# Kernel tuning notes

Hardware: AMD Instinct MI355X
Metric: run time of the kernel (lower is better)

Reference implementation:

```python
import jax, jax.numpy as jnp
import numpy as np

LN_EPS = 1e-5
BOUNDARY_ID = 0  # boundary_ids = {space_id} = {0}


def setup_inputs() -> dict:
    key = jax.random.key(0)
    k1, k2, k3 = jax.random.split(key, 3)
    B, T, D = 16, 8192, 256
    x = jax.random.normal(k1, (B, T, D), dtype=jnp.float32)
    input_ids = jax.random.randint(k2, (B, T), 0, 8, dtype=jnp.int64)
    W_proj = jax.random.normal(k3, (D, D), dtype=jnp.float32) / np.sqrt(D)
    b_proj = jnp.zeros((D,), dtype=jnp.float32)
    gamma = jnp.ones((D,), dtype=jnp.float32)
    beta = jnp.zeros((D,), dtype=jnp.float32)
    return {"x": x, "input_ids": input_ids, "W_proj": W_proj,
            "b_proj": b_proj, "gamma": gamma, "beta": beta}


def _pool(x, input_ids):
    # Boundary-defined segment mean pooling, vectorized via segment_sum.
    B, T, D = x.shape
    boundary = input_ids == BOUNDARY_ID                       # [B,T]
    nonb = ~boundary
    # A segment starts at a non-boundary token at t=0 or right after a boundary.
    prev_is_b = jnp.concatenate(
        [jnp.ones((B, 1), dtype=bool), boundary[:, :-1]], axis=1)
    start = nonb & prev_is_b
    seg = jnp.cumsum(start.astype(jnp.int32), axis=1) - 1     # seg idx per token
    MAXW = T  # static upper bound on number of segments (jit-safe padding)
    row_off = jnp.arange(B, dtype=jnp.int32)[:, None] * MAXW
    dump = B * MAXW  # boundary tokens go to a dummy segment, dropped below
    flat_ids = jnp.where(nonb, seg + row_off, dump).reshape(-1)
    sums = jax.ops.segment_sum(x.reshape(-1, D), flat_ids,
                               num_segments=B * MAXW + 1)[:-1]
    counts = jax.ops.segment_sum(jnp.ones((B * T,), x.dtype), flat_ids,
                                 num_segments=B * MAXW + 1)[:-1]
    sums = sums.reshape(B, MAXW, D)
    counts = counts.reshape(B, MAXW)
    mask = (counts > 0).astype(x.dtype)                       # [B,MAXW]
    padded = sums / jnp.maximum(counts, 1.0)[..., None]       # zeros where empty
    return padded, mask


def reference(x, input_ids, W_proj, b_proj, gamma, beta):
    padded, mask = _pool(x, input_ids)
    out = jnp.einsum('bwd,ed->bwe', padded, W_proj) + b_proj  # nn.Linear
    mu = jnp.mean(out, axis=-1, keepdims=True)
    var = jnp.mean(jnp.square(out - mu), axis=-1, keepdims=True)
    out = (out - mu) * jax.lax.rsqrt(var + LN_EPS) * gamma + beta
    return out, mask
```

## Files before the change

kernel.cpp:

```cpp
#include <hip/hip_runtime.h>
#include <hip/hip_bf16.h>
#include <math.h>

#define BB 16
#define TT 8192
#define DD 256
#define MAXSEG 4096
#define RPB 8
#define LN_EPS 1e-5f

typedef float vfloat4 __attribute__((ext_vector_type(4)));

__device__ inline float4 f4add(float4 a, float4 b) {
    a.x += b.x; a.y += b.y; a.z += b.z; a.w += b.w; return a;
}

__global__ __launch_bounds__(1024) void setup_kernel(
    const int* __restrict__ ids, const float* __restrict__ W,
    const float* __restrict__ bp, const float* __restrict__ gamma,
    const float* __restrict__ beta, int* __restrict__ counts,
    int* __restrict__ seg_start, int* __restrict__ nseg_g,
    float* __restrict__ mask_out, float* __restrict__ Wt,
    float* __restrict__ ln_empty) {
    __shared__ int wtot_s[16];
    __shared__ int wtot_n[16];
    __shared__ int segs[MAXSEG];
    __shared__ int pvals[MAXSEG];

    int tid = threadIdx.x;
    int lane = tid & 63;
    int wv = tid >> 6;

    if (blockIdx.x >= BB) {
        int bi = blockIdx.x - BB;
        if (bi < 64) {
            int d = bi * 4 + (tid >> 8);
            int e = tid & 255;
            Wt[d * DD + e] = W[e * DD + d];
        } else if (wv == 0) {
            int e0 = lane * 4;
            float4 v = *(const float4*)(bp + e0);
            float s = v.x + v.y + v.z + v.w;
            float sq = v.x * v.x + v.y * v.y + v.z * v.z + v.w * v.w;
#pragma unroll
            for (int o = 32; o > 0; o >>= 1) {
                s += __shfl_down(s, o);
                sq += __shfl_down(sq, o);
            }
            s = __shfl(s, 0);
            sq = __shfl(sq, 0);
            float mu = s * (1.f / (float)DD);
            float var = sq * (1.f / (float)DD) - mu * mu;
            float rs = rsqrtf(fmaxf(var, 0.f) + LN_EPS);
            float4 ge = *(const float4*)(gamma + e0);
            float4 be = *(const float4*)(beta + e0);
            float4 o4;
            o4.x = (v.x - mu) * rs * ge.x + be.x;
            o4.y = (v.y - mu) * rs * ge.y + be.y;
            o4.z = (v.z - mu) * rs * ge.z + be.z;
            o4.w = (v.w - mu) * rs * ge.w + be.w;
            *(float4*)(ln_empty + e0) = o4;
        }
        return;
    }

    const int TPT = 8;
    int b = blockIdx.x;
    const int* row = ids + b * TT;
    int t0 = tid * TPT;

    int4 q0 = ((const int4*)(row + t0))[0];
    int4 q1 = ((const int4*)(row + t0))[1];
    int v[TPT] = {q0.x, q0.y, q0.z, q0.w, q1.x, q1.y, q1.z, q1.w};
    int prev = (tid == 0) ? 0 : row[t0 - 1];

    bool nb[TPT], st[TPT];
    int cstart = 0, cnon = 0;
#pragma unroll
    for (int j = 0; j < TPT; ++j) {
        nb[j] = (v[j] != 0);
        int pv = (j == 0) ? prev : v[j - 1];
        st[j] = nb[j] && (pv == 0);
        cstart += st[j] ? 1 : 0;
        cnon += nb[j] ? 1 : 0;
    }

    int ss = cstart, sn = cnon;
#pragma unroll
    for (int o = 1; o < 64; o <<= 1) {
        int us = __shfl_up(ss, o);
        int un = __shfl_up(sn, o);
        if (lane >= o) { ss += us; sn += un; }
    }
    if (lane == 63) { wtot_s[wv] = ss; wtot_n[wv] = sn; }
    __syncthreads();

    int bs = 0, bn = 0, tot_s = 0, tot_n = 0;
#pragma unroll
    for (int j = 0; j < 16; ++j) {
        int a = wtot_s[j], c = wtot_n[j];
        if (j < wv) { bs += a; bn += c; }
        tot_s += a; tot_n += c;
    }
    bs += ss - cstart;
    bn += sn - cnon;

#pragma unroll
    for (int j = 0; j < TPT; ++j) {
        if (st[j]) { segs[bs] = t0 + j; pvals[bs] = bn; bs++; }
        bn += nb[j] ? 1 : 0;
    }
    __syncthreads();

    int ns = tot_s;
    for (int w = tid; w < TT; w += 1024) {
        int c = 0;
        if (w < ns) {
            int pe = (w + 1 < ns) ? pvals[w + 1] : tot_n;
            c = pe - pvals[w];
            seg_start[b * TT + w] = segs[w];
        }
        counts[b * TT + w] = c;
        mask_out[b * TT + w] = (w < ns) ? 1.0f : 0.0f;
    }
    if (tid == 0) nseg_g[b] = ns;
}

__global__ __launch_bounds__(256) void work_kernel(
    const float* __restrict__ x, const float* __restrict__ Wt,
    const float* __restrict__ bp, const float* __restrict__ gamma,
    const float* __restrict__ beta, const int* __restrict__ counts,
    const int* __restrict__ seg_start, const int* __restrict__ nseg,
    float* __restrict__ out) {
    __shared__ float pooled[RPB][DD];
    __shared__ float red[4][RPB][2];

    int b = blockIdx.x;
    int wbase = blockIdx.y * RPB;
    int ns = nseg[b];
    if (wbase >= ns) return;
    int nr = min(RPB, ns - wbase);
    int tid = threadIdx.x;
    int lane = tid & 63;
    int wv = tid >> 6;

#pragma unroll
    for (int rr = 0; rr < 2; ++rr) {
        int row = wv * 2 + rr;
        float4 a0 = {0, 0, 0, 0};
        if (row < nr) {
            int w = wbase + row;
            int s = seg_start[b * TT + w];
            int len = counts[b * TT + w];
            const float4* xp = (const float4*)(x + ((size_t)(b * TT + s)) * DD) + lane;
            float4 a1 = a0, a2 = a0, a3 = a0;
            int t = 0;
            for (; t + 4 <= len; t += 4) {
                a0 = f4add(a0, xp[(t + 0) * 64]);
                a1 = f4add(a1, xp[(t + 1) * 64]);
                a2 = f4add(a2, xp[(t + 2) * 64]);
                a3 = f4add(a3, xp[(t + 3) * 64]);
            }
            for (; t < len; ++t) a0 = f4add(a0, xp[t * 64]);
            a0 = f4add(f4add(a0, a1), f4add(a2, a3));
            float inv = 1.f / (float)len;
            a0.x *= inv; a0.y *= inv; a0.z *= inv; a0.w *= inv;
        }
        *(float4*)&pooled[row][lane * 4] = a0;
    }
    __syncthreads();

    int c = wv * 64 + lane;
    float acc[RPB];
    float bias = bp[c];
#pragma unroll
    for (int r = 0; r < RPB; ++r) acc[r] = bias;

    const float* Wc = Wt + c;
    float w0 = Wc[0 * DD];
    float w1 = Wc[1 * DD];
    float w2 = Wc[2 * DD];
    float w3 = Wc[3 * DD];
#pragma unroll 1
    for (int d0 = 0; d0 < DD; d0 += 4) {
        int dn = (d0 + 4) & 255;
        float n0 = Wc[(dn + 0) * DD];
        float n1 = Wc[(dn + 1) * DD];
        float n2 = Wc[(dn + 2) * DD];
        float n3 = Wc[(dn + 3) * DD];
#pragma unroll
        for (int r = 0; r < RPB; ++r) {
            const float4 p = *(const float4*)&pooled[r][d0];
            acc[r] = fmaf(p.x, w0, acc[r]);
            acc[r] = fmaf(p.y, w1, acc[r]);
            acc[r] = fmaf(p.z, w2, acc[r]);
            acc[r] = fmaf(p.w, w3, acc[r]);
        }
        w0 = n0; w1 = n1; w2 = n2; w3 = n3;
    }

#pragma unroll
    for (int r = 0; r < RPB; ++r) {
        float s = acc[r];
        float sq = acc[r] * acc[r];
#pragma unroll
        for (int o = 32; o > 0; o >>= 1) {
            s += __shfl_down(s, o);
            sq += __shfl_down(sq, o);
        }
        if (lane == 0) { red[wv][r][0] = s; red[wv][r][1] = sq; }
    }
    __syncthreads();

    size_t rowbase = ((size_t)(b * TT + wbase)) * DD;
    float ga = gamma[c], be = beta[c];
#pragma unroll
    for (int r = 0; r < RPB; ++r) {
        float s = red[0][r][0] + red[1][r][0] + red[2][r][0] + red[3][r][0];
        float sq = red[0][r][1] + red[1][r][1] + red[2][r][1] + red[3][r][1];
        float mu = s * (1.f / (float)DD);
        float var = sq * (1.f / (float)DD) - mu * mu;
        float rs = rsqrtf(fmaxf(var, 0.f) + LN_EPS);
        float v = (acc[r] - mu) * rs * ga + be;
        __builtin_nontemporal_store(v, out + rowbase + (size_t)r * DD + c);
    }
}

__global__ __launch_bounds__(256) void fill_kernel(const int* __restrict__ nseg,
                                                   const float* __restrict__ ln_e,
                                                   float* __restrict__ out) {
    int b = blockIdx.x;
    int wbase = blockIdx.y * RPB;
    if (wbase < nseg[b]) return;
    int tid = threadIdx.x;
    int lane = tid & 63;
    int wv = tid >> 6;
    vfloat4 lv = *(const vfloat4*)(ln_e + 4 * lane);
    float* o = out + ((size_t)(b * TT + wbase)) * DD + 4 * lane;
#pragma unroll
    for (int rr = 0; rr < 2; ++rr) {
        int row = wv * 2 + rr;
        __builtin_nontemporal_store(lv, (vfloat4*)(o + (size_t)row * DD));
    }
}

extern "C" void kernel_launch(void* const* d_in, const int* in_sizes, int n_in,
                              void* d_out, int out_size, void* d_ws, size_t ws_size,
                              hipStream_t stream) {
    const float* x = (const float*)d_in[0];
    const int* ids = (const int*)d_in[1];
    const float* W = (const float*)d_in[2];
    const float* bp = (const float*)d_in[3];
    const float* gamma = (const float*)d_in[4];
    const float* beta = (const float*)d_in[5];

    float* out = (float*)d_out;
    float* mask = out + (size_t)BB * TT * DD;

    char* ws = (char*)d_ws;
    int* counts = (int*)ws;
    int* seg_start = (int*)(ws + (size_t)BB * TT * 4);
    int* nseg = (int*)(ws + (size_t)2 * BB * TT * 4);
    float* Wt = (float*)(ws + (size_t)2 * BB * TT * 4 + 256);
    float* ln_e = Wt + DD * DD;

    hipLaunchKernelGGL(setup_kernel, dim3(BB + 64 + 1), dim3(1024), 0, stream,
                       ids, W, bp, gamma, beta, counts, seg_start, nseg, mask,
                       Wt, ln_e);
    hipLaunchKernelGGL(work_kernel, dim3(BB, TT / RPB), dim3(256), 0, stream,
                       x, Wt, bp, gamma, beta, counts, seg_start, nseg, out);
    hipLaunchKernelGGL(fill_kernel, dim3(BB, TT / RPB), dim3(256), 0, stream,
                       nseg, ln_e, out);
}
```

Before: 290.0 us.

## Split fused pool+GEMM kernel into compacted pooling and GEMM+LayerNorm kernels

The single work kernel is replaced by two kernels. A pooling kernel gives one wavefront per segment, indexed over a compacted global segment list built from per-batch segment counts, and uses 8 accumulators. A separate GEMM+LayerNorm kernel then reads the pooled rows from a workspace buffer. This packs segments densely across batches so fewer blocks exit early and the GEMM tiles are fully used. The cost is an extra global round trip for the pooled data, an additional launch, and a fixed CAP of 32768 on the total segment count.

```diff
diff --git a/kernel.cpp b/kernel.cpp
--- a/kernel.cpp
+++ b/kernel.cpp
@@ -7,6 +7,7 @@
 #define DD 256
 #define MAXSEG 4096
 #define RPB 8
+#define CAP 32768
 #define LN_EPS 1e-5f
 
 typedef float vfloat4 __attribute__((ext_vector_type(4)));
@@ -126,47 +127,79 @@
     if (tid == 0) nseg_g[b] = ns;
 }
 
-__global__ __launch_bounds__(256) void work_kernel(
-    const float* __restrict__ x, const float* __restrict__ Wt,
-    const float* __restrict__ bp, const float* __restrict__ gamma,
-    const float* __restrict__ beta, const int* __restrict__ counts,
+__device__ inline void build_offs(const int* __restrict__ nseg, int* offs,
+                                  int tid) {
+    if (tid < BB) offs[tid + 1] = nseg[tid];
+    if (tid == 0) offs[0] = 0;
+    __syncthreads();
+    if (tid == 0) {
+#pragma unroll
+        for (int b = 0; b < BB; ++b) offs[b + 1] += offs[b];
+    }
+    __syncthreads();
+}
+
+__global__ __launch_bounds__(256) void pool_kernel(
+    const float* __restrict__ x, const int* __restrict__ counts,
     const int* __restrict__ seg_start, const int* __restrict__ nseg,
-    float* __restrict__ out) {
-    __shared__ float pooled[RPB][DD];
-    __shared__ float red[4][RPB][2];
-
-    int b = blockIdx.x;
-    int wbase = blockIdx.y * RPB;
-    int ns = nseg[b];
-    if (wbase >= ns) return;
-    int nr = min(RPB, ns - wbase);
+    float* __restrict__ pooled) {
+    __shared__ int offs[BB + 1];
     int tid = threadIdx.x;
     int lane = tid & 63;
     int wv = tid >> 6;
+    build_offs(nseg, offs, tid);
+    int tot = offs[BB];
+
+    int g = blockIdx.x * 4 + wv;
+    if (g >= tot) return;
+    int b = 0;
+    while (g >= offs[b + 1]) ++b;
+    int w = g - offs[b];
+    int s = seg_start[b * TT + w];
+    int len = counts[b * TT + w];
+
+    const float4* xp = (const float4*)(x + ((size_t)(b * TT + s)) * DD) + lane;
+    float4 a[8];
+#pragma unroll
+    for (int j = 0; j < 8; ++j) a[j] = make_float4(0.f, 0.f, 0.f, 0.f);
+    int t = 0;
+    for (; t + 8 <= len; t += 8) {
+#pragma unroll
+        for (int j = 0; j < 8; ++j) a[j] = f4add(a[j], xp[(t + j) * 64]);
+    }
+    for (; t < len; ++t) a[0] = f4add(a[0], xp[t * 64]);
+    float4 r0 = f4add(f4add(a[0], a[1]), f4add(a[2], a[3]));
+    float4 r1 = f4add(f4add(a[4], a[5]), f4add(a[6], a[7]));
+    float4 r = f4add(r0, r1);
+    float inv = 1.f / (float)len;
+    r.x *= inv; r.y *= inv; r.z *= inv; r.w *= inv;
+    *(float4*)(pooled + (size_t)g * DD + 4 * lane) = r;
+}
+
+__global__ __launch_bounds__(256) void gemm_ln(
+    const float* __restrict__ pooled, const float* __restrict__ Wt,
+    const float* __restrict__ bp, const float* __restrict__ gamma,
+    const float* __restrict__ beta, const int* __restrict__ nseg,
+    float* __restrict__ out) {
+    __shared__ float pl[RPB][DD];
+    __shared__ float red[4][RPB][2];
+    __shared__ int offs[BB + 1];
+
+    int tid = threadIdx.x;
+    int lane = tid & 63;
+    int wv = tid >> 6;
+    build_offs(nseg, offs, tid);
+    int tot = offs[BB];
+    int g0 = blockIdx.x * RPB;
+    if (g0 >= tot) return;
 
 #pragma unroll
     for (int rr = 0; rr < 2; ++rr) {
-        int row = wv * 2 + rr;
-        float4 a0 = {0, 0, 0, 0};
-        if (row < nr) {
-            int w = wbase + row;
-            int s = seg_start[b * TT + w];
-            int len = counts[b * TT + w];
-            const float4* xp = (const float4*)(x + ((size_t)(b * TT + s)) * DD) + lane;
-            float4 a1 = a0, a2 = a0, a3 = a0;
-            int t = 0;
-            for (; t + 4 <= len; t += 4) {
-                a0 = f4add(a0, xp[(t + 0) * 64]);
-                a1 = f4add(a1, xp[(t + 1) * 64]);
-                a2 = f4add(a2, xp[(t + 2) * 64]);
-                a3 = f4add(a3, xp[(t + 3) * 64]);
-            }
-            for (; t < len; ++t) a0 = f4add(a0, xp[t * 64]);
-            a0 = f4add(f4add(a0, a1), f4add(a2, a3));
-            float inv = 1.f / (float)len;
-            a0.x *= inv; a0.y *= inv; a0.z *= inv; a0.w *= inv;
-        }
-        *(float4*)&pooled[row][lane * 4] = a0;
+        int r = wv * 2 + rr;
+        int g = g0 + r;
+        float4 v = make_float4(0.f, 0.f, 0.f, 0.f);
+        if (g < tot) v = *(const float4*)(pooled + (size_t)g * DD + 4 * lane);
+        *(float4*)&pl[r][lane * 4] = v;
     }
     __syncthreads();
 
@@ -190,7 +223,7 @@
         float n3 = Wc[(dn + 3) * DD];
 #pragma unroll
         for (int r = 0; r < RPB; ++r) {
-            const float4 p = *(const float4*)&pooled[r][d0];
+            const float4 p = *(const float4*)&pl[r][d0];
             acc[r] = fmaf(p.x, w0, acc[r]);
             acc[r] = fmaf(p.y, w1, acc[r]);
             acc[r] = fmaf(p.z, w2, acc[r]);
@@ -212,17 +245,22 @@
     }
     __syncthreads();
 
-    size_t rowbase = ((size_t)(b * TT + wbase)) * DD;
     float ga = gamma[c], be = beta[c];
+    int b = 0;
 #pragma unroll
     for (int r = 0; r < RPB; ++r) {
-        float s = red[0][r][0] + red[1][r][0] + red[2][r][0] + red[3][r][0];
-        float sq = red[0][r][1] + red[1][r][1] + red[2][r][1] + red[3][r][1];
-        float mu = s * (1.f / (float)DD);
-        float var = sq * (1.f / (float)DD) - mu * mu;
-        float rs = rsqrtf(fmaxf(var, 0.f) + LN_EPS);
-        float v = (acc[r] - mu) * rs * ga + be;
-        __builtin_nontemporal_store(v, out + rowbase + (size_t)r * DD + c);
+        int g = g0 + r;
+        if (g < tot) {
+            while (g >= offs[b + 1]) ++b;
+            int w = g - offs[b];
+            float s = red[0][r][0] + red[1][r][0] + red[2][r][0] + red[3][r][0];
+            float sq = red[0][r][1] + red[1][r][1] + red[2][r][1] + red[3][r][1];
+            float mu = s * (1.f / (float)DD);
+            float var = sq * (1.f / (float)DD) - mu * mu;
+            float rs = rsqrtf(fmaxf(var, 0.f) + LN_EPS);
+            float v = (acc[r] - mu) * rs * ga + be;
+            __builtin_nontemporal_store(v, out + ((size_t)(b * TT + w)) * DD + c);
+        }
     }
 }
 
@@ -263,12 +301,15 @@
     int* nseg = (int*)(ws + (size_t)2 * BB * TT * 4);
     float* Wt = (float*)(ws + (size_t)2 * BB * TT * 4 + 256);
     float* ln_e = Wt + DD * DD;
+    float* pooled = ln_e + DD;
 
     hipLaunchKernelGGL(setup_kernel, dim3(BB + 64 + 1), dim3(1024), 0, stream,
                        ids, W, bp, gamma, beta, counts, seg_start, nseg, mask,
                        Wt, ln_e);
-    hipLaunchKernelGGL(work_kernel, dim3(BB, TT / RPB), dim3(256), 0, stream,
-                       x, Wt, bp, gamma, beta, counts, seg_start, nseg, out);
+    hipLaunchKernelGGL(pool_kernel, dim3(CAP / 4), dim3(256), 0, stream,
+                       x, counts, seg_start, nseg, pooled);
+    hipLaunchKernelGGL(gemm_ln, dim3(CAP / RPB), dim3(256), 0, stream,
+                       pooled, Wt, bp, gamma, beta, nseg, out);
     hipLaunchKernelGGL(fill_kernel, dim3(BB, TT / RPB), dim3(256), 0, stream,
                        nseg, ln_e, out);
 }
```

New measurement: 307.0 us. 5.9% more time.
